# Kernel tuning notes

Measured on AMD Instinct MI355X. Metric: run time of the kernel, lower is better.

The kernel has to match this reference:

```python
import jax, jax.numpy as jnp
import numpy as np

B, T, C = 64, 256, 384
H, HD = 6, 64


def setup_inputs() -> dict:
    key = jax.random.key(0)
    ks = jax.random.split(key, 6)
    x = jax.random.normal(ks[0], (B, T, C), dtype=jnp.float32)
    s = 1.0 / np.sqrt(C)
    Wq = jax.random.normal(ks[1], (H, C, HD), dtype=jnp.float32) * s
    Wk = jax.random.normal(ks[2], (H, C, HD), dtype=jnp.float32) * s
    Wv = jax.random.normal(ks[3], (H, C, HD), dtype=jnp.float32) * s
    Wp = jax.random.normal(ks[4], (C, C), dtype=jnp.float32) * s
    bp = jnp.zeros((C,), dtype=jnp.float32)
    return {"x": x, "Wq": Wq, "Wk": Wk, "Wv": Wv, "Wp": Wp, "bp": bp}


def reference(x, Wq, Wk, Wv, Wp, bp):
    # per-head projections (no bias), vectorized over heads
    q = jnp.einsum('btc,hcd->bhtd', x, Wq)
    k = jnp.einsum('btc,hcd->bhtd', x, Wk)
    v = jnp.einsum('btc,hcd->bhtd', x, Wv)
    scale = HD ** (-0.5)
    scores = jnp.einsum('bhtd,bhsd->bhts', q, k) * scale  # [B,H,T,T]
    causal = jnp.tril(jnp.ones((T, T), dtype=bool))
    scores = jnp.where(causal, scores, -jnp.inf)
    wei = jax.nn.softmax(scores, axis=-1)  # dropout is identity in eval mode
    out = jnp.einsum('bhts,bhsd->bhtd', wei, v)
    out = out.transpose(0, 2, 1, 3).reshape(B, T, C)  # concat heads
    return out @ Wp.T + bp
```

## Files before the change

kernel.cpp:

```cpp
#include <hip/hip_runtime.h>
#include <hip/hip_bf16.h>
#include <cstdint>
#include <cstddef>

#define B_ 64
#define T_ 256
#define C_ 384
#define H_ 6
#define HD_ 64

using u16 = unsigned short;
typedef __attribute__((ext_vector_type(8))) short short8;
typedef __attribute__((ext_vector_type(4))) short short4_;
typedef __attribute__((ext_vector_type(4))) float f32x4;

__device__ __forceinline__ u16 f2bf(float f) {
    union { float f; uint32_t u; } x{f};
    uint32_t r = x.u + 0x7fffu + ((x.u >> 16) & 1u);
    return (u16)(r >> 16);
}

__global__ void k_prep(const float* __restrict__ x, const float* __restrict__ Wq,
                       const float* __restrict__ Wk, const float* __restrict__ Wv,
                       const float* __restrict__ Wp, u16* __restrict__ xb,
                       u16* __restrict__ wqkv, u16* __restrict__ wpb) {
    int bid = blockIdx.x;
    if (bid < 3072) {
        int i = (bid * 256 + threadIdx.x) * 8;
        const f32x4* p = (const f32x4*)(x + i);
        f32x4 a = p[0], b = p[1];
        short8 s;
        s[0] = (short)f2bf(a[0]); s[1] = (short)f2bf(a[1]);
        s[2] = (short)f2bf(a[2]); s[3] = (short)f2bf(a[3]);
        s[4] = (short)f2bf(b[0]); s[5] = (short)f2bf(b[1]);
        s[6] = (short)f2bf(b[2]); s[7] = (short)f2bf(b[3]);
        *(short8*)(xb + i) = s;
    } else if (bid < 3180) {
        __shared__ u16 Tt[64 * 65];
        int pb = bid - 3072;
        int which = pb / 36, rem = pb % 36;
        int h = rem / 6, cc0 = (rem % 6) * 64;
        const float* W = (which == 0) ? Wq : ((which == 1) ? Wk : Wv);
        int d = threadIdx.x & 63, cr0 = threadIdx.x >> 6;
#pragma unroll
        for (int p = 0; p < 16; ++p) {
            int cr = p * 4 + cr0;
            Tt[cr * 65 + d] = f2bf(W[(h * 384 + cc0 + cr) * 64 + d]);
        }
        __syncthreads();
        int ccl = threadIdx.x & 63, dl0 = threadIdx.x >> 6;
        int nbase = which * 384 + h * 64;
#pragma unroll
        for (int p = 0; p < 16; ++p) {
            int dl = p * 4 + dl0;
            wqkv[(size_t)(nbase + dl) * 384 + cc0 + ccl] = Tt[ccl * 65 + dl];
        }
    } else {
        int i = ((bid - 3180) * 256 + threadIdx.x) * 8;
        const f32x4* p = (const f32x4*)(Wp + i);
        f32x4 a = p[0], b = p[1];
        short8 s;
        s[0] = (short)f2bf(a[0]); s[1] = (short)f2bf(a[1]);
        s[2] = (short)f2bf(a[2]); s[3] = (short)f2bf(a[3]);
        s[4] = (short)f2bf(b[0]); s[5] = (short)f2bf(b[1]);
        s[6] = (short)f2bf(b[2]); s[7] = (short)f2bf(b[3]);
        *(short8*)(wpb + i) = s;
    }
}

__device__ __forceinline__ void stage_tile(const u16* __restrict__ gbase, int ld,
                                           u16* lds_tile, int wid, int lane, int k0) {
#pragma unroll
    for (int i = 0; i < 4; ++i) {
        int chunk = wid * 4 + i;
        int row = chunk * 8 + (lane >> 3);
        int pslot = lane & 7;
        const u16* gp = gbase + (size_t)row * ld + k0 + ((pslot ^ (row & 7)) << 3);
        u16* lp = lds_tile + chunk * 512;
        __builtin_amdgcn_global_load_lds((const __attribute__((address_space(1))) void*)gp,
                                         (__attribute__((address_space(3))) void*)lp, 16, 0, 0);
    }
}

__device__ __forceinline__ short8 read_frag(const u16* lds_tile, int row, int ks, int g) {
    int pslot = (ks * 4 + g) ^ (row & 7);
    return *(const short8*)&lds_tile[row * 64 + pslot * 8];
}

#define GEMM_PIPE_LOOP(NT)                                                        \
    int cur = 0;                                                                  \
    for (int t = 0; t < (NT); ++t) {                                              \
        if (t < (NT) - 1) {                                                       \
            stage_tile(Ag, 384, &lds[cur ^ 1][0], wid, lane, (t + 1) * 64);       \
            stage_tile(Bg, 384, &lds[cur ^ 1][8192], wid, lane, (t + 1) * 64);    \
            asm volatile("s_waitcnt vmcnt(8)" ::: "memory");                      \
        } else {                                                                  \
            asm volatile("s_waitcnt vmcnt(0)" ::: "memory");                      \
        }                                                                         \
        __builtin_amdgcn_s_barrier();                                             \
        __builtin_amdgcn_sched_barrier(0);                                        \
        const u16* A = &lds[cur][0];                                              \
        const u16* Bm = &lds[cur][8192];                                          \
        short8 af[2][4], bf[2][4];                                                \
        _Pragma("unroll")                                                         \
        for (int ks = 0; ks < 2; ++ks) {                                          \
            _Pragma("unroll")                                                     \
            for (int mf = 0; mf < 4; ++mf) af[ks][mf] = read_frag(A, wm * 64 + mf * 16 + c, ks, g); \
            _Pragma("unroll")                                                     \
            for (int nf = 0; nf < 4; ++nf) bf[ks][nf] = read_frag(Bm, wn * 64 + nf * 16 + c, ks, g); \
        }                                                                         \
        _Pragma("unroll")                                                         \
        for (int ks = 0; ks < 2; ++ks)                                            \
            _Pragma("unroll")                                                     \
            for (int mf = 0; mf < 4; ++mf)                                        \
                _Pragma("unroll")                                                 \
                for (int nf = 0; nf < 4; ++nf)                                    \
                    acc[mf][nf] = __builtin_amdgcn_mfma_f32_16x16x32_bf16(af[ks][mf], bf[ks][nf], acc[mf][nf], 0, 0, 0); \
        __builtin_amdgcn_sched_barrier(0);                                        \
        __builtin_amdgcn_s_barrier();                                             \
        cur ^= 1;                                                                 \
    }

__global__ __launch_bounds__(256, 2) void k_gemm_qkv(const u16* __restrict__ xb, const u16* __restrict__ wb,
                                                     u16* __restrict__ q, u16* __restrict__ k,
                                                     u16* __restrict__ v) {
    __shared__ alignas(16) u16 lds[2][16384];
    const int tid = threadIdx.x, lane = tid & 63, wid = tid >> 6;
    const int wm = wid >> 1, wn = wid & 1, g = lane >> 4, c = lane & 15;
    const int n0 = blockIdx.x * 128, m0 = blockIdx.y * 128;
    const u16* Ag = xb + (size_t)m0 * 384;
    const u16* Bg = wb + (size_t)n0 * 384;
    f32x4 acc[4][4] = {};
    stage_tile(Ag, 384, &lds[0][0], wid, lane, 0);
    stage_tile(Bg, 384, &lds[0][8192], wid, lane, 0);
    GEMM_PIPE_LOOP(6)
    const int which = n0 / 384;
    u16* dst = (which == 0) ? q : ((which == 1) ? k : v);
    const int h = ((n0 + wn * 64) % 384) / 64;
#pragma unroll
    for (int mf = 0; mf < 4; ++mf)
#pragma unroll
        for (int nf = 0; nf < 4; ++nf)
#pragma unroll
            for (int r = 0; r < 4; ++r) {
                int m = m0 + wm * 64 + mf * 16 + g * 4 + r;
                int d = nf * 16 + c;
                int b = m >> 8, t = m & 255;
                dst[((b * H_ + h) * T_ + t) * HD_ + d] = f2bf(acc[mf][nf][r]);
            }
}

__global__ __launch_bounds__(256, 2) void k_attn(const u16* __restrict__ q, const u16* __restrict__ k,
                                                 const u16* __restrict__ v, u16* __restrict__ ao) {
    __shared__ u16 Kt[64 * 72];
    __shared__ u16 Vt[64 * 72];
    const int tid = threadIdx.x, bh = blockIdx.x;
    const int lane = tid & 63, wid = tid >> 6;
    const int g = lane >> 4, c = lane & 15;
    const int bq = bh * 256;

    short8 qB[4][2];
#pragma unroll
    for (int qf = 0; qf < 4; ++qf)
#pragma unroll
        for (int ks = 0; ks < 2; ++ks) {
            int t = wid * 64 + qf * 16 + c;
            qB[qf][ks] = *(const short8*)&q[(bq + t) * 64 + ks * 32 + g * 8];
        }
    float mrun[4], lrun[4];
#pragma unroll
    for (int i = 0; i < 4; ++i) { mrun[i] = -1e30f; lrun[i] = 0.f; }
    f32x4 o[4][4] = {};

    for (int kt = 0; kt < 4; ++kt) {
#pragma unroll
        for (int i = 0; i < 2; ++i) {
            int idx = tid + i * 256;
            int row = idx >> 3, c8 = (idx & 7) * 8;
            *(short8*)&Kt[row * 72 + c8] = *(const short8*)&k[(bq + kt * 64 + row) * 64 + c8];
            int vrow = idx & 63, vc8 = (idx >> 6) * 8;
            int kv = ((vrow >> 5) << 5) | (((vrow >> 2) & 3) << 3) | (((vrow >> 4) & 1) << 2) | (vrow & 3);
            short8 vv = *(const short8*)&v[(bq + kt * 64 + vrow) * 64 + vc8];
#pragma unroll
            for (int j = 0; j < 8; ++j)
                Vt[(vc8 + j) * 72 + kv] = (u16)vv[j];
        }
        __syncthreads();
        if (kt <= wid) {
            f32x4 st[4][4] = {};
#pragma unroll
            for (int ks = 0; ks < 2; ++ks) {
                short8 kA[4];
#pragma unroll
                for (int sf = 0; sf < 4; ++sf)
                    kA[sf] = *(short8*)&Kt[(sf * 16 + c) * 72 + ks * 32 + g * 8];
#pragma unroll
                for (int sf = 0; sf < 4; ++sf)
#pragma unroll
                    for (int qf = 0; qf < 4; ++qf)
                        st[sf][qf] = __builtin_amdgcn_mfma_f32_16x16x32_bf16(kA[sf], qB[qf][ks], st[sf][qf], 0, 0, 0);
            }
            float pm[4] = {-1e30f, -1e30f, -1e30f, -1e30f};
#pragma unroll
            for (int sf = 0; sf < 4; ++sf)
#pragma unroll
                for (int qf = 0; qf < 4; ++qf)
#pragma unroll
                    for (int r = 0; r < 4; ++r) {
                        float val = st[sf][qf][r] * 0.125f;
                        if (kt == wid) {
                            int s_loc = sf * 16 + g * 4 + r, q_loc = qf * 16 + c;
                            if (s_loc > q_loc) val = -1e30f;
                        }
                        st[sf][qf][r] = val;
                        pm[qf] = fmaxf(pm[qf], val);
                    }
            float alpha[4];
#pragma unroll
            for (int qf = 0; qf < 4; ++qf) {
                pm[qf] = fmaxf(pm[qf], __shfl_xor(pm[qf], 16));
                pm[qf] = fmaxf(pm[qf], __shfl_xor(pm[qf], 32));
                float mnew = fmaxf(mrun[qf], pm[qf]);
                alpha[qf] = __expf(mrun[qf] - mnew);
                mrun[qf] = mnew;
            }
            short8 pA[4][2];
#pragma unroll
            for (int qf = 0; qf < 4; ++qf) {
                float ls = 0.f;
#pragma unroll
                for (int ks = 0; ks < 2; ++ks) {
                    short8 pa;
#pragma unroll
                    for (int half = 0; half < 2; ++half) {
                        f32x4 sv = st[2 * ks + half][qf];
#pragma unroll
                        for (int r = 0; r < 4; ++r) {
                            float p = __expf(sv[r] - mrun[qf]);
                            ls += p;
                            pa[half * 4 + r] = (short)f2bf(p);
                        }
                    }
                    pA[qf][ks] = pa;
                }
                ls += __shfl_xor(ls, 16);
                ls += __shfl_xor(ls, 32);
                lrun[qf] = lrun[qf] * alpha[qf] + ls;
            }
#pragma unroll
            for (int mf = 0; mf < 4; ++mf)
#pragma unroll
                for (int r = 0; r < 4; ++r) {
                    float aof = __shfl(alpha[mf], g * 4 + r);
#pragma unroll
                    for (int df = 0; df < 4; ++df)
                        o[mf][df][r] *= aof;
                }
#pragma unroll
            for (int ks = 0; ks < 2; ++ks) {
                short8 vB[4];
#pragma unroll
                for (int df = 0; df < 4; ++df)
                    vB[df] = *(short8*)&Vt[(df * 16 + c) * 72 + ks * 32 + g * 8];
#pragma unroll
                for (int mf = 0; mf < 4; ++mf)
#pragma unroll
                    for (int df = 0; df < 4; ++df)
                        o[mf][df] = __builtin_amdgcn_mfma_f32_16x16x32_bf16(pA[mf][ks], vB[df], o[mf][df], 0, 0, 0);
            }
        }
        __syncthreads();
    }
    const int bb = bh / H_, hh = bh % H_;
#pragma unroll
    for (int mf = 0; mf < 4; ++mf)
#pragma unroll
        for (int r = 0; r < 4; ++r) {
            float inv = 1.0f / __shfl(lrun[mf], g * 4 + r);
            int t = wid * 64 + mf * 16 + g * 4 + r;
#pragma unroll
            for (int df = 0; df < 4; ++df) {
                int d = df * 16 + c;
                ao[((size_t)(bb * T_ + t)) * C_ + hh * 64 + d] = f2bf(o[mf][df][r] * inv);
            }
        }
}

__global__ __launch_bounds__(256, 2) void k_gemm_proj(const u16* __restrict__ ab, const u16* __restrict__ wp,
                                                      const float* __restrict__ bp, float* __restrict__ out) {
    __shared__ alignas(16) u16 lds[2][16384];
    const int tid = threadIdx.x, lane = tid & 63, wid = tid >> 6;
    const int wm = wid >> 1, wn = wid & 1, g = lane >> 4, c = lane & 15;
    const int n0 = blockIdx.x * 128, m0 = blockIdx.y * 128;
    const u16* Ag = ab + (size_t)m0 * 384;
    const u16* Bg = wp + (size_t)n0 * 384;
    f32x4 acc[4][4] = {};
    stage_tile(Ag, 384, &lds[0][0], wid, lane, 0);
    stage_tile(Bg, 384, &lds[0][8192], wid, lane, 0);
    GEMM_PIPE_LOOP(6)
#pragma unroll
    for (int mf = 0; mf < 4; ++mf)
#pragma unroll
        for (int nf = 0; nf < 4; ++nf)
#pragma unroll
            for (int r = 0; r < 4; ++r) {
                int m = m0 + wm * 64 + mf * 16 + g * 4 + r;
                int n = n0 + wn * 64 + nf * 16 + c;
                out[(size_t)m * C_ + n] = acc[mf][nf][r] + bp[n];
            }
}


extern "C" void kernel_launch(void* const* d_in, const int* in_sizes, int n_in,
                              void* d_out, int out_size, void* d_ws, size_t ws_size,
                              hipStream_t stream) {
    const float* x  = (const float*)d_in[0];
    const float* Wq = (const float*)d_in[1];
    const float* Wk = (const float*)d_in[2];
    const float* Wv = (const float*)d_in[3];
    const float* Wp = (const float*)d_in[4];
    const float* bp = (const float*)d_in[5];
    float* out = (float*)d_out;

    char* ws = (char*)d_ws;
    u16* xb   = (u16*)(ws);
    u16* wqkv = (u16*)(ws + 12582912);
    u16* wpb  = (u16*)(ws + 13467648);
    u16* qb   = (u16*)(ws + 13762560);
    u16* kb   = (u16*)(ws + 26345472);
    u16* vb   = (u16*)(ws + 38928384);
    u16* ab   = (u16*)(ws + 51511296);

    k_prep<<<3252, 256, 0, stream>>>(x, Wq, Wk, Wv, Wp, xb, wqkv, wpb);
    k_gemm_qkv<<<dim3(9, 128), 256, 0, stream>>>(xb, wqkv, qb, kb, vb);
    k_attn<<<384, 256, 0, stream>>>(qb, kb, vb, ab);
    k_gemm_proj<<<dim3(3, 128), 256, 0, stream>>>(ab, wpb, bp, out);
}
```

Before: 74.09 us.

## Double-buffer K/V tiles in attention with async LDS loads and prefetch

The attention kernel now double-buffers K and V in shared memory. The next K tile is prefetched through global_load_lds into a swizzled layout, and the next V tile is loaded into registers during compute and written transposed to LDS (4x4 short4 transposes) after the MFMAs, so there is one barrier per iteration instead of two. MFMA sections are also wrapped in s_setprio. This is meant to hide global-load latency behind compute, at the cost of doubled LDS use that may reduce occupancy. No vmcnt wait is visible before the barrier for the async K loads, so correctness depends on the barrier or compiler inserting one.

```diff
diff --git a/kernel.cpp b/kernel.cpp
--- a/kernel.cpp
+++ b/kernel.cpp
@@ -68,11 +68,12 @@
     }
 }
 
-__device__ __forceinline__ void stage_tile(const u16* __restrict__ gbase, int ld,
+template<int NROWS>
+__device__ __forceinline__ void stage_rows(const u16* __restrict__ gbase, int ld,
                                            u16* lds_tile, int wid, int lane, int k0) {
 #pragma unroll
-    for (int i = 0; i < 4; ++i) {
-        int chunk = wid * 4 + i;
+    for (int i = 0; i < NROWS / 32; ++i) {
+        int chunk = wid * (NROWS / 32) + i;
         int row = chunk * 8 + (lane >> 3);
         int pslot = lane & 7;
         const u16* gp = gbase + (size_t)row * ld + k0 + ((pslot ^ (row & 7)) << 3);
@@ -80,6 +81,11 @@
         __builtin_amdgcn_global_load_lds((const __attribute__((address_space(1))) void*)gp,
                                          (__attribute__((address_space(3))) void*)lp, 16, 0, 0);
     }
+}
+
+__device__ __forceinline__ void stage_tile(const u16* __restrict__ gbase, int ld,
+                                           u16* lds_tile, int wid, int lane, int k0) {
+    stage_rows<128>(gbase, ld, lds_tile, wid, lane, k0);
 }
 
 __device__ __forceinline__ short8 read_frag(const u16* lds_tile, int row, int ks, int g) {
@@ -152,13 +158,17 @@
 
 __global__ __launch_bounds__(256, 2) void k_attn(const u16* __restrict__ q, const u16* __restrict__ k,
                                                  const u16* __restrict__ v, u16* __restrict__ ao) {
-    __shared__ u16 Kt[64 * 72];
-    __shared__ u16 Vt[64 * 72];
+    __shared__ alignas(16) u16 Kl[2][64 * 64];
+    __shared__ alignas(16) u16 Vt[2][64][72];
     const int tid = threadIdx.x, bh = blockIdx.x;
     const int lane = tid & 63, wid = tid >> 6;
     const int g = lane >> 4, c = lane & 15;
     const int bq = bh * 256;
 
+    const int vd0 = (tid & 15) * 4;
+    const int vs0 = (tid >> 4) * 4;
+    const int kb0 = ((vs0 >> 5) << 5) | (((vs0 >> 2) & 3) << 3) | (((vs0 >> 4) & 1) << 2);
+
     short8 qB[4][2];
 #pragma unroll
     for (int qf = 0; qf < 4; ++qf)
@@ -172,34 +182,44 @@
     for (int i = 0; i < 4; ++i) { mrun[i] = -1e30f; lrun[i] = 0.f; }
     f32x4 o[4][4] = {};
 
+    short4_ vv[4];
+    stage_rows<64>(k + (size_t)(bq) * 64, 64, &Kl[0][0], wid, lane, 0);
+#pragma unroll
+    for (int i = 0; i < 4; ++i)
+        vv[i] = *(const short4_*)&v[(size_t)(bq + vs0 + i) * 64 + vd0];
+#pragma unroll
+    for (int j = 0; j < 4; ++j) {
+        short4_ w4;
+#pragma unroll
+        for (int i = 0; i < 4; ++i) w4[i] = vv[i][j];
+        *(short4_*)&Vt[0][vd0 + j][kb0] = w4;
+    }
+    __syncthreads();
+
+    int buf = 0;
     for (int kt = 0; kt < 4; ++kt) {
-#pragma unroll
-        for (int i = 0; i < 2; ++i) {
-            int idx = tid + i * 256;
-            int row = idx >> 3, c8 = (idx & 7) * 8;
-            *(short8*)&Kt[row * 72 + c8] = *(const short8*)&k[(bq + kt * 64 + row) * 64 + c8];
-            int vrow = idx & 63, vc8 = (idx >> 6) * 8;
-            int kv = ((vrow >> 5) << 5) | (((vrow >> 2) & 3) << 3) | (((vrow >> 4) & 1) << 2) | (vrow & 3);
-            short8 vv = *(const short8*)&v[(bq + kt * 64 + vrow) * 64 + vc8];
-#pragma unroll
-            for (int j = 0; j < 8; ++j)
-                Vt[(vc8 + j) * 72 + kv] = (u16)vv[j];
-        }
-        __syncthreads();
+        if (kt < 3) {
+            stage_rows<64>(k + (size_t)(bq + (kt + 1) * 64) * 64, 64, &Kl[buf ^ 1][0], wid, lane, 0);
+#pragma unroll
+            for (int i = 0; i < 4; ++i)
+                vv[i] = *(const short4_*)&v[(size_t)(bq + (kt + 1) * 64 + vs0 + i) * 64 + vd0];
+        }
         if (kt <= wid) {
             f32x4 st[4][4] = {};
+            __builtin_amdgcn_s_setprio(1);
 #pragma unroll
             for (int ks = 0; ks < 2; ++ks) {
                 short8 kA[4];
 #pragma unroll
                 for (int sf = 0; sf < 4; ++sf)
-                    kA[sf] = *(short8*)&Kt[(sf * 16 + c) * 72 + ks * 32 + g * 8];
+                    kA[sf] = read_frag(&Kl[buf][0], sf * 16 + c, ks, g);
 #pragma unroll
                 for (int sf = 0; sf < 4; ++sf)
 #pragma unroll
                     for (int qf = 0; qf < 4; ++qf)
                         st[sf][qf] = __builtin_amdgcn_mfma_f32_16x16x32_bf16(kA[sf], qB[qf][ks], st[sf][qf], 0, 0, 0);
             }
+            __builtin_amdgcn_s_setprio(0);
             float pm[4] = {-1e30f, -1e30f, -1e30f, -1e30f};
 #pragma unroll
             for (int sf = 0; sf < 4; ++sf)
@@ -256,20 +276,32 @@
                     for (int df = 0; df < 4; ++df)
                         o[mf][df][r] *= aof;
                 }
+            __builtin_amdgcn_s_setprio(1);
 #pragma unroll
             for (int ks = 0; ks < 2; ++ks) {
                 short8 vB[4];
 #pragma unroll
                 for (int df = 0; df < 4; ++df)
-                    vB[df] = *(short8*)&Vt[(df * 16 + c) * 72 + ks * 32 + g * 8];
+                    vB[df] = *(short8*)&Vt[buf][df * 16 + c][ks * 32 + g * 8];
 #pragma unroll
                 for (int mf = 0; mf < 4; ++mf)
 #pragma unroll
                     for (int df = 0; df < 4; ++df)
                         o[mf][df] = __builtin_amdgcn_mfma_f32_16x16x32_bf16(pA[mf][ks], vB[df], o[mf][df], 0, 0, 0);
             }
+            __builtin_amdgcn_s_setprio(0);
+        }
+        if (kt < 3) {
+#pragma unroll
+            for (int j = 0; j < 4; ++j) {
+                short4_ w4;
+#pragma unroll
+                for (int i = 0; i < 4; ++i) w4[i] = vv[i][j];
+                *(short4_*)&Vt[buf ^ 1][vd0 + j][kb0] = w4;
+            }
         }
         __syncthreads();
+        buf ^= 1;
     }
     const int bb = bh / H_, hh = bh % H_;
 #pragma unroll
```

Result: no change. 73.52 us (-0.8%).
